# Optimization experiments

Measured on AMD Instinct MI355X. Metric: run time of the kernel, lower is better.

The kernel has to match this reference:

```python
import jax, jax.numpy as jnp
import numpy as np

B, T, C, HS = 1024, 256, 384, 64

def setup_inputs() -> dict:
    key = jax.random.key(0)
    kx, kq, kk, kv = jax.random.split(key, 4)
    x = jax.random.normal(kx, (B, T, C), dtype=jnp.float32)
    # torch Linear(no bias): y = x @ W.T with W [hs, C]; store transposed [C, hs]
    s = 1.0 / np.sqrt(C)
    Wq = jax.random.uniform(kq, (C, HS), jnp.float32, -s, s)
    Wk = jax.random.uniform(kk, (C, HS), jnp.float32, -s, s)
    Wv = jax.random.uniform(kv, (C, HS), jnp.float32, -s, s)
    return {"x": x, "Wq": Wq, "Wk": Wk, "Wv": Wv}

def reference(x, Wq, Wk, Wv):
    Tn = x.shape[1]
    hs = Wq.shape[1]
    q = x @ Wq  # [B,T,hs]
    k = x @ Wk
    v = x @ Wv
    scores = jnp.einsum('bqd,bkd->bqk', q, k) * (hs ** -0.5)  # [B,T,T]
    causal = jnp.tril(jnp.ones((Tn, Tn), dtype=bool))
    scores = jnp.where(causal[None, :, :], scores, -jnp.inf)
    wei = jax.nn.softmax(scores, axis=-1)
    out = jnp.einsum('bqk,bkd->bqd', wei, v)  # [B,T,hs]
    return out
```

## Files before the change

kernel.cpp:

```cpp
#include <hip/hip_runtime.h>
#include <hip/hip_bf16.h>

#define TT 256
#define CC 384
#define HSZ 64

typedef __attribute__((ext_vector_type(8))) short bf16x8;
typedef __attribute__((ext_vector_type(4))) float f32x4;

static __device__ __forceinline__ unsigned short f2bf(float f) {
    union { __hip_bfloat16 h; unsigned short u; } cv;
    cv.h = __float2bfloat16(f);
    return cv.u;
}

static __device__ __forceinline__ bf16x8 cvt8(float4 a, float4 b) {
    bf16x8 r;
    r[0] = (short)f2bf(a.x); r[1] = (short)f2bf(a.y);
    r[2] = (short)f2bf(a.z); r[3] = (short)f2bf(a.w);
    r[4] = (short)f2bf(b.x); r[5] = (short)f2bf(b.y);
    r[6] = (short)f2bf(b.z); r[7] = (short)f2bf(b.w);
    return r;
}

__global__ __launch_bounds__(256) void wtrans_kernel(
        const float* __restrict__ Wq,
        const float* __restrict__ Wk,
        const float* __restrict__ Wv,
        unsigned short* __restrict__ Wt) {
    int idx = blockIdx.x * 256 + threadIdx.x;
    if (idx >= 192 * CC) return;
    int n = idx / CC;
    int ck = idx - n * CC;
    const float* W = (n < 64) ? Wq : ((n < 128) ? Wk : Wv);
    Wt[n * CC + ck] = f2bf(W[ck * HSZ + (n & 63)]);
}

__global__ __launch_bounds__(512, 2) void fused_kernel(
        const float* __restrict__ x,
        const unsigned short* __restrict__ Wt,
        float* __restrict__ outp) {
    __shared__ __align__(16) unsigned short k_lds[TT][72];
    __shared__ __align__(16) unsigned short v_lds[HSZ][264];
    __shared__ __align__(16) unsigned short pbuf[8][16][40];

    const int b    = blockIdx.x;
    const int lane = threadIdx.x & 63;
    const int w    = threadIdx.x >> 6;
    const int c    = lane & 15;
    const int quad = lane >> 4;

    const int Rl0 = 16 * w;
    const int Rl1 = 240 - 16 * w;

    f32x4 acc[2][12];
    #pragma unroll
    for (int t = 0; t < 2; ++t)
        #pragma unroll
        for (int n = 0; n < 12; ++n)
            acc[t][n] = (f32x4){0.f, 0.f, 0.f, 0.f};

    const float* xa0 = x + ((size_t)b * TT + Rl0 + c) * CC + quad * 8;
    const float* xa1 = x + ((size_t)b * TT + Rl1 + c) * CC + quad * 8;
    const unsigned short* wb = Wt + c * CC + quad * 8;

    float4 A0lo = *(const float4*)(xa0);
    float4 A0hi = *(const float4*)(xa0 + 4);
    float4 A1lo = *(const float4*)(xa1);
    float4 A1hi = *(const float4*)(xa1 + 4);
    float4 B0lo = *(const float4*)(xa0 + 32);
    float4 B0hi = *(const float4*)(xa0 + 36);
    float4 B1lo = *(const float4*)(xa1 + 32);
    float4 B1hi = *(const float4*)(xa1 + 36);

    #pragma unroll
    for (int s = 0; s < 12; ++s) {
        bf16x8 a0 = cvt8(A0lo, A0hi);
        bf16x8 a1 = cvt8(A1lo, A1hi);
        A0lo = B0lo; A0hi = B0hi; A1lo = B1lo; A1hi = B1hi;
        if (s < 10) {
            B0lo = *(const float4*)(xa0 + (s + 2) * 32);
            B0hi = *(const float4*)(xa0 + (s + 2) * 32 + 4);
            B1lo = *(const float4*)(xa1 + (s + 2) * 32);
            B1hi = *(const float4*)(xa1 + (s + 2) * 32 + 4);
        }
        #pragma unroll
        for (int n = 0; n < 12; ++n) {
            bf16x8 bfv = *(const bf16x8*)(wb + n * 16 * CC + s * 32);
            acc[0][n] = __builtin_amdgcn_mfma_f32_16x16x32_bf16(a0, bfv, acc[0][n], 0, 0, 0);
            acc[1][n] = __builtin_amdgcn_mfma_f32_16x16x32_bf16(a1, bfv, acc[1][n], 0, 0, 0);
        }
    }

    bf16x8 qf[2][2];
    #pragma unroll
    for (int t = 0; t < 2; ++t) {
        const int lr = (t == 0 ? Rl0 : Rl1) + quad * 4;
        #pragma unroll
        for (int n = 4; n < 8; ++n) {
            const int cg = (n - 4) * 16 + c;
            #pragma unroll
            for (int r = 0; r < 4; ++r)
                k_lds[lr + r][cg] = f2bf(acc[t][n][r]);
        }
        #pragma unroll
        for (int n = 8; n < 12; ++n) {
            const int hsg = (n - 8) * 16 + c;
            ushort4 pk;
            pk.x = f2bf(acc[t][n][0]);
            pk.y = f2bf(acc[t][n][1]);
            pk.z = f2bf(acc[t][n][2]);
            pk.w = f2bf(acc[t][n][3]);
            *(ushort4*)(&v_lds[hsg][lr]) = pk;
        }
        #pragma unroll
        for (int p = 0; p < 2; ++p) {
            #pragma unroll
            for (int n2 = 0; n2 < 2; ++n2) {
                const int n = 2 * p + n2;
                #pragma unroll
                for (int r = 0; r < 4; ++r)
                    pbuf[w][quad * 4 + r][n2 * 16 + c] = f2bf(acc[t][n][r]);
            }
            qf[t][p] = *(const bf16x8*)(&pbuf[w][c][quad * 8]);
        }
    }

    __syncthreads();

    const int mt0 = w;
    const int mt1 = 15 - w;

    f32x4 of[2][4];
    float mst[2] = {-1e30f, -1e30f};
    float lst[2] = {0.f, 0.f};
    #pragma unroll
    for (int i = 0; i < 2; ++i)
        #pragma unroll
        for (int n = 0; n < 4; ++n)
            of[i][n] = (f32x4){0.f, 0.f, 0.f, 0.f};

    const float qscale = 0.18033688011112042f;

    for (int kt = 0; kt < 8; ++kt) {
        if (mt1 < 2 * kt) break;
        const int k0 = kt * 32;

        bf16x8 kf[2][2], vf[4];
        #pragma unroll
        for (int nt = 0; nt < 2; ++nt)
            #pragma unroll
            for (int ks = 0; ks < 2; ++ks)
                kf[nt][ks] = *(const bf16x8*)(&k_lds[k0 + nt * 16 + c][ks * 32 + quad * 8]);
        #pragma unroll
        for (int n = 0; n < 4; ++n)
            vf[n] = *(const bf16x8*)(&v_lds[n * 16 + c][k0 + quad * 8]);

        #pragma unroll
        for (int ti = 0; ti < 2; ++ti) {
            const int mt = ti ? mt1 : mt0;
            if (mt < 2 * kt) continue;
            const int rb = mt * 16;

            f32x4 s0 = {0.f, 0.f, 0.f, 0.f}, s1 = {0.f, 0.f, 0.f, 0.f};
            #pragma unroll
            for (int ks = 0; ks < 2; ++ks) {
                s0 = __builtin_amdgcn_mfma_f32_16x16x32_bf16(kf[0][ks], qf[ti][ks], s0, 0, 0, 0);
                s1 = __builtin_amdgcn_mfma_f32_16x16x32_bf16(kf[1][ks], qf[ti][ks], s1, 0, 0, 0);
            }

            float t0[4], t1[4];
            #pragma unroll
            for (int r = 0; r < 4; ++r) { t0[r] = s0[r] * qscale; t1[r] = s1[r] * qscale; }

            if (mt < 2 * kt + 2) {
                #pragma unroll
                for (int r = 0; r < 4; ++r) {
                    const int kk = k0 + quad * 4 + r;
                    if (kk > rb + c)      t0[r] = -1e30f;
                    if (kk + 16 > rb + c) t1[r] = -1e30f;
                }
            }

            float mx = fmaxf(fmaxf(fmaxf(t0[0], t0[1]), fmaxf(t0[2], t0[3])),
                             fmaxf(fmaxf(t1[0], t1[1]), fmaxf(t1[2], t1[3])));
            mx = fmaxf(mx, __shfl_xor(mx, 16, 64));
            mx = fmaxf(mx, __shfl_xor(mx, 32, 64));

            const float mnew  = fmaxf(mst[ti], mx);
            const float alpha = exp2f(mst[ti] - mnew);
            mst[ti] = mnew;

            float p0[4], p1[4];
            float rs = 0.f;
            #pragma unroll
            for (int r = 0; r < 4; ++r) {
                p0[r] = exp2f(t0[r] - mnew);
                p1[r] = exp2f(t1[r] - mnew);
                rs += p0[r] + p1[r];
            }
            rs += __shfl_xor(rs, 16, 64);
            rs += __shfl_xor(rs, 32, 64);
            lst[ti] = lst[ti] * alpha + rs;

            #pragma unroll
            for (int n = 0; n < 4; ++n)
                #pragma unroll
                for (int r = 0; r < 4; ++r)
                    of[ti][n][r] *= alpha;

            ushort4 pk0, pk1;
            pk0.x = f2bf(p0[0]); pk0.y = f2bf(p0[1]); pk0.z = f2bf(p0[2]); pk0.w = f2bf(p0[3]);
            pk1.x = f2bf(p1[0]); pk1.y = f2bf(p1[1]); pk1.z = f2bf(p1[2]); pk1.w = f2bf(p1[3]);
            *(ushort4*)(&pbuf[w][c][quad * 4])      = pk0;
            *(ushort4*)(&pbuf[w][c][16 + quad * 4]) = pk1;
            bf16x8 pf = *(const bf16x8*)(&pbuf[w][c][quad * 8]);

            #pragma unroll
            for (int n = 0; n < 4; ++n)
                of[ti][n] = __builtin_amdgcn_mfma_f32_16x16x32_bf16(vf[n], pf, of[ti][n], 0, 0, 0);
        }
    }

    float* ob = outp + (size_t)b * TT * HSZ;
    #pragma unroll
    for (int ti = 0; ti < 2; ++ti) {
        const int rb = (ti ? mt1 : mt0) * 16;
        const float inv = 1.f / lst[ti];
        #pragma unroll
        for (int n = 0; n < 4; ++n) {
            float4 st;
            st.x = of[ti][n][0] * inv;
            st.y = of[ti][n][1] * inv;
            st.z = of[ti][n][2] * inv;
            st.w = of[ti][n][3] * inv;
            *(float4*)(ob + (size_t)(rb + c) * HSZ + n * 16 + quad * 4) = st;
        }
    }
}

extern "C" void kernel_launch(void* const* d_in, const int* in_sizes, int n_in,
                              void* d_out, int out_size, void* d_ws, size_t ws_size,
                              hipStream_t stream) {
    const float* x  = (const float*)d_in[0];
    const float* Wq = (const float*)d_in[1];
    const float* Wk = (const float*)d_in[2];
    const float* Wv = (const float*)d_in[3];
    float* outp = (float*)d_out;

    const int Bn = in_sizes[0] / (TT * CC);

    unsigned short* Wt = (unsigned short*)d_ws;

    hipLaunchKernelGGL(wtrans_kernel, dim3(288), dim3(256), 0, stream, Wq, Wk, Wv, Wt);
    hipLaunchKernelGGL(fused_kernel, dim3(Bn), dim3(512), 0, stream, x, Wt, outp);
}
```

Measured before the change: 665.9 us.

## Stage projection weights into double-buffered swizzled LDS via global_load_lds

```diff
diff --git a/kernel.cpp b/kernel.cpp
--- a/kernel.cpp
+++ b/kernel.cpp
@@ -40,6 +40,7 @@
         const float* __restrict__ x,
         const unsigned short* __restrict__ Wt,
         float* __restrict__ outp) {
+    __shared__ __align__(16) unsigned short wtb[2][192][64];
     __shared__ __align__(16) unsigned short k_lds[TT][72];
     __shared__ __align__(16) unsigned short v_lds[HSZ][264];
     __shared__ __align__(16) unsigned short pbuf[8][16][40];
@@ -53,6 +54,36 @@
     const int Rl0 = 16 * w;
     const int Rl1 = 240 - 16 * w;
 
+    auto stage_wt = [&](int g) {
+        unsigned short* dst = &wtb[g & 1][0][0];
+        #pragma unroll
+        for (int i = 0; i < 3; ++i) {
+            const int base = w * 3072 + i * 1024;
+            const int off  = base + lane * 16;
+            const int row  = off >> 7;
+            const int P    = (off >> 4) & 7;
+            const unsigned short* src = Wt + row * CC + g * 64 + ((P ^ (row & 7)) * 8);
+            __builtin_amdgcn_global_load_lds(
+                (const __attribute__((address_space(1))) unsigned int*)(const void*)src,
+                (__attribute__((address_space(3))) unsigned int*)(void*)(dst + (base >> 1)),
+                16, 0, 0);
+        }
+    };
+
+    const float* xa0 = x + ((size_t)b * TT + Rl0 + c) * CC + quad * 8;
+    const float* xa1 = x + ((size_t)b * TT + Rl1 + c) * CC + quad * 8;
+
+    stage_wt(0);
+
+    float4 X[3][4];
+    #pragma unroll
+    for (int i = 0; i < 3; ++i) {
+        X[i][0] = *(const float4*)(xa0 + i * 32);
+        X[i][1] = *(const float4*)(xa0 + i * 32 + 4);
+        X[i][2] = *(const float4*)(xa1 + i * 32);
+        X[i][3] = *(const float4*)(xa1 + i * 32 + 4);
+    }
+
     f32x4 acc[2][12];
     #pragma unroll
     for (int t = 0; t < 2; ++t)
@@ -60,33 +91,28 @@
         for (int n = 0; n < 12; ++n)
             acc[t][n] = (f32x4){0.f, 0.f, 0.f, 0.f};
 
-    const float* xa0 = x + ((size_t)b * TT + Rl0 + c) * CC + quad * 8;
-    const float* xa1 = x + ((size_t)b * TT + Rl1 + c) * CC + quad * 8;
-    const unsigned short* wb = Wt + c * CC + quad * 8;
-
-    float4 A0lo = *(const float4*)(xa0);
-    float4 A0hi = *(const float4*)(xa0 + 4);
-    float4 A1lo = *(const float4*)(xa1);
-    float4 A1hi = *(const float4*)(xa1 + 4);
-    float4 B0lo = *(const float4*)(xa0 + 32);
-    float4 B0hi = *(const float4*)(xa0 + 36);
-    float4 B1lo = *(const float4*)(xa1 + 32);
-    float4 B1hi = *(const float4*)(xa1 + 36);
+    __syncthreads();
 
     #pragma unroll
     for (int s = 0; s < 12; ++s) {
-        bf16x8 a0 = cvt8(A0lo, A0hi);
-        bf16x8 a1 = cvt8(A1lo, A1hi);
-        A0lo = B0lo; A0hi = B0hi; A1lo = B1lo; A1hi = B1hi;
-        if (s < 10) {
-            B0lo = *(const float4*)(xa0 + (s + 2) * 32);
-            B0hi = *(const float4*)(xa0 + (s + 2) * 32 + 4);
-            B1lo = *(const float4*)(xa1 + (s + 2) * 32);
-            B1hi = *(const float4*)(xa1 + (s + 2) * 32 + 4);
-        }
+        if (s >= 2 && (s & 1) == 0) __syncthreads();
+        if ((s & 1) == 0 && s <= 8) stage_wt(s / 2 + 1);
+
+        bf16x8 a0 = cvt8(X[s % 3][0], X[s % 3][1]);
+        bf16x8 a1 = cvt8(X[s % 3][2], X[s % 3][3]);
+        if (s + 3 < 12) {
+            X[s % 3][0] = *(const float4*)(xa0 + (s + 3) * 32);
+            X[s % 3][1] = *(const float4*)(xa0 + (s + 3) * 32 + 4);
+            X[s % 3][2] = *(const float4*)(xa1 + (s + 3) * 32);
+            X[s % 3][3] = *(const float4*)(xa1 + (s + 3) * 32 + 4);
+        }
+
+        const int g = s >> 1, p = s & 1;
         #pragma unroll
         for (int n = 0; n < 12; ++n) {
-            bf16x8 bfv = *(const bf16x8*)(wb + n * 16 * CC + s * 32);
+            const int row  = n * 16 + c;
+            const int slot = (p * 4 + quad) ^ (c & 7);
+            bf16x8 bfv = *(const bf16x8*)(&wtb[g & 1][row][slot * 8]);
             acc[0][n] = __builtin_amdgcn_mfma_f32_16x16x32_bf16(a0, bfv, acc[0][n], 0, 0, 0);
             acc[1][n] = __builtin_amdgcn_mfma_f32_16x16x32_bf16(a1, bfv, acc[1][n], 0, 0, 0);
         }
```

Measured after the change: 577.0 us. -13.3%, faster.
